# Optimization experiments

Measured on AMD Instinct MI355X. Metric: run time of the kernel, lower is better.

## Reference

```python
import jax, jax.numpy as jnp
import numpy as np

# ---- static config (mirrors module init / config constants) ----
STATE_DIM = 512
D_H = 2048
INPUT_DIM = 1024
N_QUBITS = 6
N_VQC_LAYERS = 3
MSD = 128                 # mamba_state_dim (last dim of padded state)
PAD_SLICES = 16           # padded slice count in h_padded
MIN_T = 1e-6              # control_limits.min_value
REL_STEP = 0.1            # control_limits.hardware_relative_step
ABS_STEP = 1e-4           # control_limits.hardware_absolute_step
MAX_T = 0.05              # control_limits.max_value
DIM = 2 ** N_QUBITS

# qubit 0 = most significant bit (matches reshape-based gate application)
_BITS = ((np.arange(DIM)[:, None] >> np.arange(N_QUBITS)[None, ::-1]) & 1).astype(np.float32)
_sign = np.ones(DIM, np.float32)
for k in range(N_QUBITS):  # ring CZ entanglement
    k2 = (k + 1) % N_QUBITS
    _sign *= 1.0 - 2.0 * _BITS[:, k] * _BITS[:, k2]
CZ_SIGN = jnp.asarray(_sign)
Z_OBS = jnp.asarray((1.0 - 2.0 * _BITS).mean(axis=1))  # mean <Z_k> observable weights


def _apply_ry(state, ang, k):
    # state: [B, 2^n] real statevector; ang: [B] rotation angle on qubit k
    B = state.shape[0]
    s = state.reshape(B, 2 ** k, 2, 2 ** (N_QUBITS - k - 1))
    c = jnp.cos(ang / 2)[:, None, None]
    si = jnp.sin(ang / 2)[:, None, None]
    a0, a1 = s[:, :, 0, :], s[:, :, 1, :]
    out = jnp.stack([c * a0 - si * a1, si * a0 + c * a1], axis=2)
    return out.reshape(B, DIM)


def _vqc(feats, enc_W, enc_b, thetas):
    # EvolutionTimeVQCLayer: angle-encode features, layered RY + ring CZ, mean-Z expectation
    B = feats.shape[0]
    angles = feats @ enc_W + enc_b  # [B, n_qubits]
    state = jnp.zeros((B, DIM), feats.dtype).at[:, 0].set(1.0)
    for k in range(N_QUBITS):
        state = _apply_ry(state, angles[:, k], k)
    for l in range(N_VQC_LAYERS):
        for k in range(N_QUBITS):
            state = _apply_ry(state, jnp.broadcast_to(thetas[l, k], (B,)), k)
        state = state * CZ_SIGN[None, :]
    return (state * state) @ Z_OBS  # [B]


def _hamiltonian(q, p, x, W1, b1, W2, b2, W3, b3):
    z = jnp.concatenate([q, p, x], axis=-1)          # [B, 2*S + D]
    h1 = jnp.tanh(z @ W1 + b1)
    h2 = jnp.tanh(h1 @ W2 + b2)
    return (h2 @ W3)[:, 0] + b3                       # [B] scalar energy per sample


def setup_inputs() -> dict:
    key = jax.random.key(0)
    ks = jax.random.split(key, 12)
    def glorot(k, shape):
        std = np.sqrt(2.0 / (shape[0] + shape[-1]))
        return jax.random.normal(k, shape, jnp.float32) * std
    B = 2048
    h_in = 2 * STATE_DIM + INPUT_DIM
    gen_in = INPUT_DIM + 2 * STATE_DIM
    return {
        'x': jax.random.normal(ks[0], (B, INPUT_DIM), jnp.float32),
        'h_padded': jax.random.normal(ks[1], (B, PAD_SLICES, MSD), jnp.float32),
        'aux_padded': jnp.zeros((B, PAD_SLICES, MSD), jnp.float32),
        'W1': glorot(ks[2], (h_in, D_H)), 'b1': jnp.zeros((D_H,), jnp.float32),
        'W2': glorot(ks[3], (D_H, D_H)), 'b2': jnp.zeros((D_H,), jnp.float32),
        'W3': glorot(ks[4], (D_H, 1)), 'b3': jnp.zeros((), jnp.float32),
        'W_out': glorot(ks[5], (2 * STATE_DIM, INPUT_DIM)),
        'b_out': jnp.zeros((INPUT_DIM,), jnp.float32),
        'enc_W': glorot(ks[6], (gen_in, N_QUBITS)) * 0.1,
        'enc_b': jnp.zeros((N_QUBITS,), jnp.float32),
        'thetas': jax.random.normal(ks[7], (N_VQC_LAYERS, N_QUBITS), jnp.float32) * 0.1,
        'gain': jnp.asarray(0.1, jnp.float32),
        'shift': jnp.asarray(7.0, jnp.float32),
        'cap_param': jnp.asarray(0.02, jnp.float32),
        'time_bias': jnp.asarray(0.0005, jnp.float32),
        'last_stable': jnp.asarray(0.0005, jnp.float32),
    }


def reference(x, h_padded, aux_padded, W1, b1, W2, b2, W3, b3, W_out, b_out,
              enc_W, enc_b, thetas, gain, shift, cap_param, time_bias, last_stable):
    B = x.shape[0]
    total = 2 * STATE_DIM
    num_slices = total // MSD
    # unpack phase-space state from padded mamba-shaped state
    unpacked = h_padded[:, :num_slices, :].reshape(B, total)
    q_t, p_t = jnp.split(unpacked, 2, axis=-1)

    # ---- evolution-time generation via VQC ----
    ctrl = jnp.concatenate([x, q_t, p_t], axis=-1)
    samples = _vqc(ctrl, enc_W, enc_b, thetas)                       # [B]
    soft_gain = jax.nn.softplus(gain)
    soft_shift = jax.nn.softplus(shift)
    adjusted = jax.nn.softplus(soft_gain * samples - soft_shift)
    raw = jnp.mean(adjusted) + time_bias
    cap = jnp.maximum(jax.nn.softplus(cap_param), 1e-6)
    evo = cap * jax.nn.sigmoid(raw / cap)
    evo = jnp.where(jnp.isfinite(evo), evo, cap * jax.nn.sigmoid(time_bias / cap))
    prev = jnp.maximum(last_stable, MIN_T)
    cand = jnp.maximum(evo, MIN_T)
    max_step = jnp.maximum(prev * REL_STEP, ABS_STEP)
    cand = jnp.minimum(cand, prev + max_step)
    cand = jnp.minimum(cand, MAX_T)
    dt = jnp.where(jnp.isfinite(cand), cand, prev)                   # scalar

    # ---- fused HNN symplectic (leapfrog) step ----
    def H_sum(q, p):
        return _hamiltonian(q, p, x, W1, b1, W2, b2, W3, b3).sum()
    grad_qp = jax.grad(H_sum, argnums=(0, 1))
    dHdq0, _ = grad_qp(q_t, p_t)
    p_half = p_t - 0.5 * dt * dHdq0
    _, dHdp_h = grad_qp(q_t, p_half)
    q_next = q_t + dt * dHdp_h
    dHdq_n, _ = grad_qp(q_next, p_half)
    p_next = p_half - 0.5 * dt * dHdq_n

    out = jnp.concatenate([q_next, p_next], axis=-1) @ W_out + b_out  # [B, INPUT_DIM]

    # repack state into padded mamba layout
    new_slices = jnp.concatenate([q_next, p_next], axis=-1).reshape(B, num_slices, MSD)
    pad = jnp.zeros((B, PAD_SLICES - num_slices, MSD), out.dtype)
    h_next = jnp.concatenate([new_slices, pad], axis=1)
    return out, h_next
```

## Files before the change

kernel.cpp:

```cpp
#include <hip/hip_runtime.h>
#include <math.h>

#define NB 2048
#define ZD 2048
#define SD 512
#define NELEM_Z (NB * ZD)
#define MB_ (1024 * 1024)

typedef float f32x4 __attribute__((ext_vector_type(4)));
typedef __bf16 bf16x8 __attribute__((ext_vector_type(8)));
typedef __bf16 bf16x4 __attribute__((ext_vector_type(4)));
typedef int i32x4 __attribute__((ext_vector_type(4)));
typedef int i32x8 __attribute__((ext_vector_type(8)));
typedef long long i64;

__device__ __forceinline__ float softplus_f(float x) {
  if (x > 20.f) return x;
  if (x < -20.f) return expf(x);
  return log1pf(expf(x));
}

__device__ __forceinline__ void gload_lds16(const __bf16* g, __bf16* l) {
  __builtin_amdgcn_global_load_lds(
      (__attribute__((address_space(1))) void*)(g),
      (__attribute__((address_space(3))) void*)(l), 16, 0, 0);
}

__device__ __forceinline__ int pack_fp8x4(float a, float b, float c, float d) {
  int p = __builtin_amdgcn_cvt_pk_fp8_f32(a, b, 0, false);
  p = __builtin_amdgcn_cvt_pk_fp8_f32(c, d, p, true);
  return p;
}
__device__ __forceinline__ float fp8_to_f32(unsigned char b) {
  return __builtin_amdgcn_cvt_f32_fp8((int)b, 0);
}

__global__ __launch_bounds__(256) void build_z_kernel(
    const float* __restrict__ x,
    const float* __restrict__ h_padded,
    const float* __restrict__ enc_W,
    const float* __restrict__ enc_b,
    float* __restrict__ z,
    __bf16* __restrict__ zb,
    unsigned char* __restrict__ zf8,
    float* __restrict__ angles) {
  int b = blockIdx.x;
  int tid = threadIdx.x;
  int lane = tid & 63, w = tid >> 6;
  __shared__ float red[4][6];

  float pa[6] = {0.f, 0.f, 0.f, 0.f, 0.f, 0.f};
#pragma unroll
  for (int cc = 0; cc < 2; cc++) {
    int c = cc * 256 + tid;
    int i = c * 4;
    f32x4 v = (i < 1024) ? ((const f32x4*)(h_padded + (size_t)b * 2048))[c]
                         : ((const f32x4*)(x + (size_t)b * 1024))[c - 256];
    size_t zi = (size_t)b * 512 + c;
    ((f32x4*)z)[zi] = v;
    bf16x4 o;
    o[0] = (__bf16)v[0]; o[1] = (__bf16)v[1];
    o[2] = (__bf16)v[2]; o[3] = (__bf16)v[3];
    ((bf16x4*)zb)[zi] = o;
    ((int*)zf8)[zi] = pack_fp8x4(v[0], v[1], v[2], v[3]);
    int cj = (i < 1024) ? (1024 + i) : (i - 1024);
#pragma unroll
    for (int e = 0; e < 4; e++) {
      const float* wp = enc_W + (size_t)(cj + e) * 6;
#pragma unroll
      for (int k = 0; k < 6; k++) pa[k] += v[e] * wp[k];
    }
  }
#pragma unroll
  for (int k = 0; k < 6; k++)
    for (int off = 32; off > 0; off >>= 1) pa[k] += __shfl_down(pa[k], off, 64);
  if (lane == 0) {
#pragma unroll
    for (int k = 0; k < 6; k++) red[w][k] = pa[k];
  }
  __syncthreads();
  if (tid < 6)
    angles[b * 6 + tid] =
        red[0][tid] + red[1][tid] + red[2][tid] + red[3][tid] + enc_b[tid];
}

__global__ void prep_w(const float* __restrict__ in,
                       __bf16* __restrict__ outT, int R, int C) {
  __shared__ float tile[32][33];
  int bx = blockIdx.x * 32, by = blockIdx.y * 32;
  int tx = threadIdx.x, ty = threadIdx.y;
  for (int r = ty; r < 32; r += 8)
    tile[r][tx] = in[(size_t)(by + r) * C + bx + tx];
  __syncthreads();
  for (int r = ty; r < 32; r += 8)
    outT[(size_t)(bx + r) * R + by + tx] = (__bf16)tile[tx][r];
}

__global__ void prep_w8(const float* __restrict__ in,
                        unsigned char* __restrict__ outN,
                        unsigned char* __restrict__ outT, int R, int C) {
  __shared__ float tile[32][33];
  int bx = blockIdx.x * 32, by = blockIdx.y * 32;
  int tx = threadIdx.x, ty = threadIdx.y;
  for (int r = ty; r < 32; r += 8) {
    float v = in[(size_t)(by + r) * C + bx + tx] * 16.f;
    tile[r][tx] = v;
    int p = __builtin_amdgcn_cvt_pk_fp8_f32(v, v, 0, false);
    outN[(size_t)(by + r) * C + bx + tx] = (unsigned char)(p & 0xff);
  }
  __syncthreads();
  for (int r = ty; r < 32; r += 8) {
    float v = tile[tx][r];
    int p = __builtin_amdgcn_cvt_pk_fp8_f32(v, v, 0, false);
    outT[(size_t)(bx + r) * R + by + tx] = (unsigned char)(p & 0xff);
  }
}

__global__ __launch_bounds__(256) void sim_kernel(
    const float* __restrict__ angles,
    const float* __restrict__ thetas,
    const float* __restrict__ gain,
    const float* __restrict__ shift,
    float* __restrict__ partial) {
  const int lane = threadIdx.x & 63;
  const int wv = threadIdx.x >> 6;
  const int row = blockIdx.x * 4 + wv;

  const int rot = ((lane << 1) | (lane >> 5)) & 63;
  const float czs = (__popc(lane & rot) & 1) ? -1.f : 1.f;
  const float zo = (6.f - 2.f * (float)__popc(lane)) * (1.f / 6.f);

  float ang = 0.f;
  if (lane < 6) ang = angles[row * 6 + lane];
  else if (lane < 24) ang = thetas[lane - 6];
  float half = 0.5f * ang;
  float cj = cosf(half), sj = sinf(half);

  float c_arr[24], s_arr[24];
#pragma unroll
  for (int j = 0; j < 24; j++) {
    c_arr[j] = __shfl(cj, j, 64);
    s_arr[j] = __shfl(sj, j, 64);
  }

  float s = (lane == 0) ? 1.f : 0.f;
#pragma unroll
  for (int j = 0; j < 24; j++) {
    const int m = 1 << (5 - (j % 6));
    float t = __shfl_xor(s, m, 64);
    float tt = (lane & m) ? t : -t;
    s = fmaf(c_arr[j], s, s_arr[j] * tt);
    if (j >= 6 && (j % 6) == 5) s *= czs;
  }

  float val = s * s * zo;
#pragma unroll
  for (int off = 32; off > 0; off >>= 1) val += __shfl_xor(val, off, 64);

  __shared__ float red[4];
  if (lane == 0) {
    float sg = softplus_f(gain[0]);
    float ss = softplus_f(shift[0]);
    red[wv] = softplus_f(sg * val - ss);
  }
  __syncthreads();
  if (threadIdx.x == 0)
    partial[blockIdx.x] = red[0] + red[1] + red[2] + red[3];
}

__global__ __launch_bounds__(256) void dt_kernel(
    const float* __restrict__ partial,
    const float* __restrict__ cap_param,
    const float* __restrict__ time_bias,
    const float* __restrict__ last_stable,
    float* __restrict__ dt_out) {
  int tid = threadIdx.x;
  int lane = tid & 63, wv = tid >> 6;
  float v = partial[tid] + partial[tid + 256];
#pragma unroll
  for (int off = 32; off > 0; off >>= 1) v += __shfl_xor(v, off, 64);
  __shared__ float red[4];
  if (lane == 0) red[wv] = v;
  __syncthreads();
  if (tid == 0) {
    float a = red[0] + red[1] + red[2] + red[3];
    float raw = a * (1.f / (float)NB) + time_bias[0];
    float cap = fmaxf(softplus_f(cap_param[0]), 1e-6f);
    float evo = cap / (1.f + expf(-raw / cap));
    if (!isfinite(evo)) evo = cap / (1.f + expf(-time_bias[0] / cap));
    float prev = fmaxf(last_stable[0], 1e-6f);
    float cand = fmaxf(evo, 1e-6f);
    float max_step = fmaxf(prev * 0.1f, 1e-4f);
    cand = fminf(cand, prev + max_step);
    cand = fminf(cand, 0.05f);
    dt_out[0] = isfinite(cand) ? cand : prev;
  }
}

template <int EPI>
__global__ __launch_bounds__(256, 2) void mfma_gemm8(
    const unsigned char* __restrict__ A, int lda,
    const unsigned char* __restrict__ Bt, int ldb,
    void* __restrict__ Cv, int ldc,
    const float* __restrict__ bias,
    const float* __restrict__ w3,
    const unsigned char* __restrict__ aux, int ldaux,
    int Kslice) {
  __shared__ __align__(16) unsigned char sA[2][128 * 128];
  __shared__ __align__(16) unsigned char sB[2][64 * 128];

  const int tid = threadIdx.x;
  const int lane = tid & 63;
  const int w = tid >> 6;
  const int wm = w & 1, wn = w >> 1;
  const int row0 = blockIdx.y * 128;
  const int col0 = blockIdx.x * 64;
  const int koff = blockIdx.z * Kslice;

  const unsigned char* gA[4]; int wA[4];
  const unsigned char* gB[2]; int wB[2];
#pragma unroll
  for (int i = 0; i < 4; i++) {
    int c = i * 256 + tid;
    int m = c >> 3, s = c & 7;
    gA[i] = A + (size_t)(row0 + m) * lda + koff + s * 16;
    wA[i] = m * 128 + ((s ^ (m & 7)) << 4);
  }
#pragma unroll
  for (int i = 0; i < 2; i++) {
    int c = i * 256 + tid;
    int m = c >> 3, s = c & 7;
    gB[i] = Bt + (size_t)(col0 + m) * ldb + koff + s * 16;
    wB[i] = m * 128 + ((s ^ (m & 7)) << 4);
  }

  const int q = lane >> 4, r = lane & 15;
  int aoff[4][2], boff[2][2];
#pragma unroll
  for (int i = 0; i < 4; i++) {
    int ma = wm * 64 + i * 16 + r;
#pragma unroll
    for (int H = 0; H < 2; H++)
      aoff[i][H] = ma * 128 + (((2 * q + H) ^ (ma & 7)) << 4);
  }
#pragma unroll
  for (int j = 0; j < 2; j++) {
    int mb = wn * 32 + j * 16 + r;
#pragma unroll
    for (int H = 0; H < 2; H++)
      boff[j][H] = mb * 128 + (((2 * q + H) ^ (mb & 7)) << 4);
  }

  f32x4 acc[4][2] = {};
  f32x4 rA[4], rB[2];

#pragma unroll
  for (int i = 0; i < 4; i++) rA[i] = *(const f32x4*)gA[i];
#pragma unroll
  for (int i = 0; i < 2; i++) rB[i] = *(const f32x4*)gB[i];
#pragma unroll
  for (int i = 0; i < 4; i++) *(f32x4*)(&sA[0][0] + wA[i]) = rA[i];
#pragma unroll
  for (int i = 0; i < 2; i++) *(f32x4*)(&sB[0][0] + wB[i]) = rB[i];
  __syncthreads();

  int cur = 0;
  for (int k0 = 0; k0 < Kslice; k0 += 128) {
    const bool more = (k0 + 128 < Kslice);
    if (more) {
#pragma unroll
      for (int i = 0; i < 4; i++) rA[i] = *(const f32x4*)(gA[i] + k0 + 128);
#pragma unroll
      for (int i = 0; i < 2; i++) rB[i] = *(const f32x4*)(gB[i] + k0 + 128);
    }

    const unsigned char* bA = &sA[cur][0];
    const unsigned char* bB = &sB[cur][0];
    i32x8 af[4], bfr[2];
#pragma unroll
    for (int i = 0; i < 4; i++) {
      i32x4 lo = *(const i32x4*)(bA + aoff[i][0]);
      i32x4 hi = *(const i32x4*)(bA + aoff[i][1]);
      af[i] = __builtin_shufflevector(lo, hi, 0, 1, 2, 3, 4, 5, 6, 7);
    }
#pragma unroll
    for (int j = 0; j < 2; j++) {
      i32x4 lo = *(const i32x4*)(bB + boff[j][0]);
      i32x4 hi = *(const i32x4*)(bB + boff[j][1]);
      bfr[j] = __builtin_shufflevector(lo, hi, 0, 1, 2, 3, 4, 5, 6, 7);
    }
#pragma unroll
    for (int i = 0; i < 4; i++)
#pragma unroll
      for (int j = 0; j < 2; j++)
        acc[i][j] = __builtin_amdgcn_mfma_scale_f32_16x16x128_f8f6f4(
            af[i], bfr[j], acc[i][j], 0 , 0 ,
            0, 0x7F7F7F7F, 0, 0x7F7F7F7F);

    if (more) {
      unsigned char* nA = &sA[cur ^ 1][0];
      unsigned char* nB = &sB[cur ^ 1][0];
#pragma unroll
      for (int i = 0; i < 4; i++) *(f32x4*)(nA + wA[i]) = rA[i];
#pragma unroll
      for (int i = 0; i < 2; i++) *(f32x4*)(nB + wB[i]) = rB[i];
    }
    __syncthreads();
    cur ^= 1;
  }

  float* Cf = (float*)Cv;
  unsigned char* C8 = (unsigned char*)Cv;
  float* Pz = Cf + (size_t)blockIdx.z * (size_t)gridDim.y * 128 * ldc;

#pragma unroll
  for (int i = 0; i < 4; i++) {
    int rowb = row0 + wm * 64 + i * 16 + q * 4;
#pragma unroll
    for (int j = 0; j < 2; j++) {
      int col = col0 + wn * 32 + j * 16 + r;
      if (EPI == 0) {
#pragma unroll
        for (int g = 0; g < 4; g++)
          Pz[(size_t)(rowb + g) * ldc + col] = acc[i][j][g];
      } else {
        float o[4];
#pragma unroll
        for (int g = 0; g < 4; g++) {
          float v = acc[i][j][g] * 0.0625f;
          if (EPI == 1) {
            o[g] = tanhf(v + bias[col]);
          } else if (EPI == 2) {
            float t = tanhf(v + bias[col]);
            o[g] = 32.f * (1.f - t * t) * w3[col];
          } else {
            float h = fp8_to_f32(aux[(size_t)(rowb + g) * ldaux + col]);
            o[g] = v * (1.f - h * h);
          }
        }
        int p = pack_fp8x4(o[0], o[1], o[2], o[3]);
#pragma unroll
        for (int g = 0; g < 4; g++)
          C8[(size_t)(rowb + g) * ldc + col] =
              (unsigned char)((p >> (8 * g)) & 0xff);
      }
    }
  }
}

__global__ __launch_bounds__(256, 2) void mfma_gemm_bf16(
    const __bf16* __restrict__ A, int lda,
    const __bf16* __restrict__ Bt, int ldb,
    float* __restrict__ P, int ldc,
    int Kslice) {
  __shared__ __bf16 sA[2][128 * 64];
  __shared__ __bf16 sB[2][64 * 64];

  const int tid = threadIdx.x;
  const int lane = tid & 63;
  const int w = tid >> 6;
  const int wm = w & 1, wn = w >> 1;
  const int row0 = blockIdx.y * 128;
  const int col0 = blockIdx.x * 64;
  const int koff = blockIdx.z * Kslice;

  const __bf16* gA[4]; int lofA[4];
  const __bf16* gB[2]; int lofB[2];
#pragma unroll
  for (int i = 0; i < 4; i++) {
    int c = i * 256 + tid;
    int m = c >> 3, cc = c & 7;
    int o = cc ^ (m & 7);
    gA[i] = A + (size_t)(row0 + m) * lda + koff + o * 8;
    lofA[i] = c * 8;
  }
#pragma unroll
  for (int i = 0; i < 2; i++) {
    int c = i * 256 + tid;
    int m = c >> 3, cc = c & 7;
    int o = cc ^ (m & 7);
    gB[i] = Bt + (size_t)(col0 + m) * ldb + koff + o * 8;
    lofB[i] = c * 8;
  }

  const int q = lane >> 4, r = lane & 15;
  int aoff[4][2], boff[2][2];
#pragma unroll
  for (int i = 0; i < 4; i++) {
    int ma = wm * 64 + i * 16 + r;
#pragma unroll
    for (int h = 0; h < 2; h++)
      aoff[i][h] = (ma * 8 + ((h * 4 + q) ^ (ma & 7))) * 8;
  }
#pragma unroll
  for (int j = 0; j < 2; j++) {
    int mb = wn * 32 + j * 16 + r;
#pragma unroll
    for (int h = 0; h < 2; h++)
      boff[j][h] = (mb * 8 + ((h * 4 + q) ^ (mb & 7))) * 8;
  }

  f32x4 acc[4][2] = {};

#pragma unroll
  for (int i = 0; i < 4; i++) gload_lds16(gA[i], &sA[0][0] + lofA[i]);
#pragma unroll
  for (int i = 0; i < 2; i++) gload_lds16(gB[i], &sB[0][0] + lofB[i]);

  int cur = 0;
  for (int k0 = 0; k0 < Kslice; k0 += 64) {
    __syncthreads();
    if (k0 + 64 < Kslice) {
      int nxt = cur ^ 1;
#pragma unroll
      for (int i = 0; i < 4; i++)
        gload_lds16(gA[i] + k0 + 64, &sA[nxt][0] + lofA[i]);
#pragma unroll
      for (int i = 0; i < 2; i++)
        gload_lds16(gB[i] + k0 + 64, &sB[nxt][0] + lofB[i]);
    }
#pragma unroll
    for (int h = 0; h < 2; h++) {
      bf16x8 af[4], bfr[2];
#pragma unroll
      for (int i = 0; i < 4; i++)
        af[i] = *(const bf16x8*)(&sA[cur][0] + aoff[i][h]);
#pragma unroll
      for (int j = 0; j < 2; j++)
        bfr[j] = *(const bf16x8*)(&sB[cur][0] + boff[j][h]);
#pragma unroll
      for (int i = 0; i < 4; i++)
#pragma unroll
        for (int j = 0; j < 2; j++)
          acc[i][j] = __builtin_amdgcn_mfma_f32_16x16x32_bf16(af[i], bfr[j],
                                                              acc[i][j], 0, 0, 0);
    }
    cur ^= 1;
  }

  float* Pz = P + (size_t)blockIdx.z * (size_t)gridDim.y * 128 * ldc;
#pragma unroll
  for (int i = 0; i < 4; i++) {
    int rowb = row0 + wm * 64 + i * 16 + q * 4;
#pragma unroll
    for (int j = 0; j < 2; j++) {
      int col = col0 + wn * 32 + j * 16 + r;
#pragma unroll
      for (int g = 0; g < 4; g++)
        Pz[(size_t)(rowb + g) * ldc + col] = acc[i][j][g];
    }
  }
}

__global__ void update_kernel(float* __restrict__ z, __bf16* __restrict__ zb,
                              unsigned char* __restrict__ zf8,
                              const float* __restrict__ gp,
                              const float* __restrict__ dt,
                              float coef, int off) {
  int t = blockIdx.x * blockDim.x + threadIdx.x;
  int b = t >> 7;
  int j4 = t & 127;
  const f32x4* g4 = (const f32x4*)gp;
  constexpr int STRIDE = NB * SD / 4;
  f32x4 g = g4[t] + g4[t + STRIDE] + g4[t + 2 * STRIDE] + g4[t + 3 * STRIDE];
  int zi4 = (b * ZD + off) / 4 + j4;
  f32x4 v = ((f32x4*)z)[zi4];
  float s = coef * dt[0] * (1.f / 512.f);
  v[0] += s * g[0]; v[1] += s * g[1]; v[2] += s * g[2]; v[3] += s * g[3];
  ((f32x4*)z)[zi4] = v;
  bf16x4 o;
  o[0] = (__bf16)v[0]; o[1] = (__bf16)v[1];
  o[2] = (__bf16)v[2]; o[3] = (__bf16)v[3];
  ((bf16x4*)zb)[zi4] = o;
  ((int*)zf8)[zi4] = pack_fp8x4(v[0], v[1], v[2], v[3]);
}

__global__ void wout_reduce(const float* __restrict__ gp,
                            const float* __restrict__ b_out,
                            float* __restrict__ out) {
  int t = blockIdx.x * blockDim.x + threadIdx.x;
  constexpr int S = NB * 1024 / 4;
  const f32x4* g4 = (const f32x4*)gp;
  f32x4 v = g4[t] + g4[t + S];
  f32x4 bb = ((const f32x4*)b_out)[t & 255];
  v[0] += bb[0]; v[1] += bb[1]; v[2] += bb[2]; v[3] += bb[3];
  ((f32x4*)out)[t] = v;
}

__global__ void hnext_kernel(const float* __restrict__ z,
                             float* __restrict__ out) {
  int t = blockIdx.x * blockDim.x + threadIdx.x;
  int i4 = t & 511;
  f32x4 zero = {0.f, 0.f, 0.f, 0.f};
  ((f32x4*)out)[t] = (i4 < 256) ? ((const f32x4*)z)[t] : zero;
}

extern "C" void kernel_launch(void* const* d_in, const int* in_sizes, int n_in,
                              void* d_out, int out_size, void* d_ws,
                              size_t ws_size, hipStream_t stream) {
  const float* x        = (const float*)d_in[0];
  const float* h_padded = (const float*)d_in[1];
  const float* W1    = (const float*)d_in[3];
  const float* b1    = (const float*)d_in[4];
  const float* W2    = (const float*)d_in[5];
  const float* b2    = (const float*)d_in[6];
  const float* W3    = (const float*)d_in[7];
  const float* W_out = (const float*)d_in[9];
  const float* b_out = (const float*)d_in[10];
  const float* enc_W = (const float*)d_in[11];
  const float* enc_b = (const float*)d_in[12];
  const float* thetas = (const float*)d_in[13];
  const float* gain   = (const float*)d_in[14];
  const float* shift  = (const float*)d_in[15];
  const float* cap_p  = (const float*)d_in[16];
  const float* t_bias = (const float*)d_in[17];
  const float* l_stab = (const float*)d_in[18];

  float* out_mat  = (float*)d_out;
  float* out_hnxt = (float*)d_out + NB * 1024;

  char* base = (char*)d_ws;
  float* z      = (float*)(base);
  float* part   = (float*)(base + 16 * MB_);
  __bf16* zb    = (__bf16*)(base + 32 * MB_);
  __bf16* Wot   = (__bf16*)(base + 40 * MB_);
  float* angl   = (float*)(base + 42 * MB_);
  float* accp   = (float*)(base + 42 * MB_ + 65536);
  float* dtp    = accp + 1;
  float* simp   = (float*)(base + 42 * MB_ + 80 * 1024);
  unsigned char* zf8  = (unsigned char*)(base + 43 * MB_);
  unsigned char* h1_8 = zf8 + (size_t)NELEM_Z;
  unsigned char* g2_8 = h1_8 + (size_t)NELEM_Z;
  unsigned char* g1_8 = g2_8 + (size_t)NELEM_Z;
  unsigned char* W1n8 = g1_8 + (size_t)NELEM_Z;
  unsigned char* W1t8 = W1n8 + (size_t)NELEM_Z;
  unsigned char* W2n8 = W1t8 + (size_t)NELEM_Z;
  unsigned char* W2t8 = W2n8 + (size_t)NELEM_Z;

  dim3 thr256(256);
  dim3 thrT(32, 8);

  prep_w8<<<dim3(64, 64), thrT, 0, stream>>>(W1, W1n8, W1t8, ZD, ZD);
  prep_w8<<<dim3(64, 64), thrT, 0, stream>>>(W2, W2n8, W2t8, ZD, ZD);
  prep_w<<<dim3(32, 32), thrT, 0, stream>>>(W_out, Wot, 1024, 1024);

  build_z_kernel<<<dim3(NB), thr256, 0, stream>>>(x, h_padded, enc_W, enc_b, z,
                                                  zb, zf8, angl);
  sim_kernel<<<dim3(NB / 4), thr256, 0, stream>>>(angl, thetas, gain, shift,
                                                  simp);
  dt_kernel<<<dim3(1), thr256, 0, stream>>>(simp, cap_p, t_bias, l_stab, dtp);

  const int   j0r[3]  = {0, 512, 0};
  const int   offs[3] = {512, 0, 512};
  const float coef[3] = {-0.5f, 1.0f, -0.5f};

  dim3 gridSq(32, 16, 1);
  dim3 gridGr(8, 16, 4);

  for (int i = 0; i < 3; i++) {
    mfma_gemm8<1><<<gridSq, thr256, 0, stream>>>(
        zf8, ZD, W1t8, ZD, h1_8, ZD, b1, nullptr, nullptr, 0, ZD);
    mfma_gemm8<2><<<gridSq, thr256, 0, stream>>>(
        h1_8, ZD, W2t8, ZD, g2_8, ZD, b2, W3, nullptr, 0, ZD);
    mfma_gemm8<3><<<gridSq, thr256, 0, stream>>>(
        g2_8, ZD, W2n8, ZD, g1_8, ZD, nullptr, nullptr, h1_8, ZD, ZD);
    mfma_gemm8<0><<<gridGr, thr256, 0, stream>>>(
        g1_8, ZD, W1n8 + (size_t)j0r[i] * ZD, ZD, part, SD, nullptr, nullptr,
        nullptr, 0, 512);
    update_kernel<<<dim3(NB * SD / 4 / 256), thr256, 0, stream>>>(
        z, zb, zf8, part, dtp, coef[i], offs[i]);
  }

  mfma_gemm_bf16<<<dim3(16, 16, 2), thr256, 0, stream>>>(zb, ZD, Wot, 1024,
                                                         part, 1024, 512);
  wout_reduce<<<dim3(NB * 1024 / 4 / 256), thr256, 0, stream>>>(part, b_out,
                                                                out_mat);

  hnext_kernel<<<dim3(NELEM_Z / 4 / 256), thr256, 0, stream>>>(z, out_hnxt);
}
```

Baseline: 412.1 us.

## Widen FP8 GEMM tile to 128x128 and stage operands with direct global-to-LDS loads

The FP8 MFMA GEMM tile grows from 128x64 to 128x128 outputs per block, so each wave computes a 4x4 grid of 16x16 MFMA tiles and operand reuse improves. Launch grids are halved to match. Global-to-register-to-LDS staging is replaced by global_load_lds direct copies, with the XOR swizzle moved to the global source address, and the barrier moved to the top of the loop. The costs are twice the LDS per block, more accumulator registers, and only about one block per CU, which may leave little latency hiding.

```diff
diff --git a/kernel.cpp b/kernel.cpp
--- a/kernel.cpp
+++ b/kernel.cpp
@@ -21,6 +21,12 @@
 }
 
 __device__ __forceinline__ void gload_lds16(const __bf16* g, __bf16* l) {
+  __builtin_amdgcn_global_load_lds(
+      (__attribute__((address_space(1))) void*)(g),
+      (__attribute__((address_space(3))) void*)(l), 16, 0, 0);
+}
+__device__ __forceinline__ void gload_lds16u(const unsigned char* g,
+                                             unsigned char* l) {
   __builtin_amdgcn_global_load_lds(
       (__attribute__((address_space(1))) void*)(g),
       (__attribute__((address_space(3))) void*)(l), 16, 0, 0);
@@ -207,35 +213,31 @@
     const unsigned char* __restrict__ aux, int ldaux,
     int Kslice) {
   __shared__ __align__(16) unsigned char sA[2][128 * 128];
-  __shared__ __align__(16) unsigned char sB[2][64 * 128];
+  __shared__ __align__(16) unsigned char sB[2][128 * 128];
 
   const int tid = threadIdx.x;
   const int lane = tid & 63;
   const int w = tid >> 6;
   const int wm = w & 1, wn = w >> 1;
   const int row0 = blockIdx.y * 128;
-  const int col0 = blockIdx.x * 64;
+  const int col0 = blockIdx.x * 128;
   const int koff = blockIdx.z * Kslice;
 
-  const unsigned char* gA[4]; int wA[4];
-  const unsigned char* gB[2]; int wB[2];
+  const unsigned char* gA[4];
+  const unsigned char* gB[4];
+  int ldst[4];
 #pragma unroll
   for (int i = 0; i < 4; i++) {
     int c = i * 256 + tid;
     int m = c >> 3, s = c & 7;
-    gA[i] = A + (size_t)(row0 + m) * lda + koff + s * 16;
-    wA[i] = m * 128 + ((s ^ (m & 7)) << 4);
-  }
-#pragma unroll
-  for (int i = 0; i < 2; i++) {
-    int c = i * 256 + tid;
-    int m = c >> 3, s = c & 7;
-    gB[i] = Bt + (size_t)(col0 + m) * ldb + koff + s * 16;
-    wB[i] = m * 128 + ((s ^ (m & 7)) << 4);
+    int l = s ^ (m & 7);
+    gA[i] = A + (size_t)(row0 + m) * lda + koff + l * 16;
+    gB[i] = Bt + (size_t)(col0 + m) * ldb + koff + l * 16;
+    ldst[i] = c * 16;
   }
 
   const int q = lane >> 4, r = lane & 15;
-  int aoff[4][2], boff[2][2];
+  int aoff[4][2], boff[4][2];
 #pragma unroll
   for (int i = 0; i < 4; i++) {
     int ma = wm * 64 + i * 16 + r;
@@ -244,39 +246,36 @@
       aoff[i][H] = ma * 128 + (((2 * q + H) ^ (ma & 7)) << 4);
   }
 #pragma unroll
-  for (int j = 0; j < 2; j++) {
-    int mb = wn * 32 + j * 16 + r;
+  for (int j = 0; j < 4; j++) {
+    int mb = wn * 64 + j * 16 + r;
 #pragma unroll
     for (int H = 0; H < 2; H++)
       boff[j][H] = mb * 128 + (((2 * q + H) ^ (mb & 7)) << 4);
   }
 
-  f32x4 acc[4][2] = {};
-  f32x4 rA[4], rB[2];
-
-#pragma unroll
-  for (int i = 0; i < 4; i++) rA[i] = *(const f32x4*)gA[i];
-#pragma unroll
-  for (int i = 0; i < 2; i++) rB[i] = *(const f32x4*)gB[i];
-#pragma unroll
-  for (int i = 0; i < 4; i++) *(f32x4*)(&sA[0][0] + wA[i]) = rA[i];
-#pragma unroll
-  for (int i = 0; i < 2; i++) *(f32x4*)(&sB[0][0] + wB[i]) = rB[i];
-  __syncthreads();
+  f32x4 acc[4][4] = {};
+
+#pragma unroll
+  for (int i = 0; i < 4; i++) gload_lds16u(gA[i], &sA[0][0] + ldst[i]);
+#pragma unroll
+  for (int i = 0; i < 4; i++) gload_lds16u(gB[i], &sB[0][0] + ldst[i]);
 
   int cur = 0;
   for (int k0 = 0; k0 < Kslice; k0 += 128) {
-    const bool more = (k0 + 128 < Kslice);
-    if (more) {
-#pragma unroll
-      for (int i = 0; i < 4; i++) rA[i] = *(const f32x4*)(gA[i] + k0 + 128);
-#pragma unroll
-      for (int i = 0; i < 2; i++) rB[i] = *(const f32x4*)(gB[i] + k0 + 128);
+    __syncthreads();
+    if (k0 + 128 < Kslice) {
+      int nxt = cur ^ 1;
+#pragma unroll
+      for (int i = 0; i < 4; i++)
+        gload_lds16u(gA[i] + k0 + 128, &sA[nxt][0] + ldst[i]);
+#pragma unroll
+      for (int i = 0; i < 4; i++)
+        gload_lds16u(gB[i] + k0 + 128, &sB[nxt][0] + ldst[i]);
     }
 
     const unsigned char* bA = &sA[cur][0];
     const unsigned char* bB = &sB[cur][0];
-    i32x8 af[4], bfr[2];
+    i32x8 af[4], bfr[4];
 #pragma unroll
     for (int i = 0; i < 4; i++) {
       i32x4 lo = *(const i32x4*)(bA + aoff[i][0]);
@@ -284,7 +283,7 @@
       af[i] = __builtin_shufflevector(lo, hi, 0, 1, 2, 3, 4, 5, 6, 7);
     }
 #pragma unroll
-    for (int j = 0; j < 2; j++) {
+    for (int j = 0; j < 4; j++) {
       i32x4 lo = *(const i32x4*)(bB + boff[j][0]);
       i32x4 hi = *(const i32x4*)(bB + boff[j][1]);
       bfr[j] = __builtin_shufflevector(lo, hi, 0, 1, 2, 3, 4, 5, 6, 7);
@@ -292,20 +291,10 @@
 #pragma unroll
     for (int i = 0; i < 4; i++)
 #pragma unroll
-      for (int j = 0; j < 2; j++)
+      for (int j = 0; j < 4; j++)
         acc[i][j] = __builtin_amdgcn_mfma_scale_f32_16x16x128_f8f6f4(
             af[i], bfr[j], acc[i][j], 0 , 0 ,
             0, 0x7F7F7F7F, 0, 0x7F7F7F7F);
-
-    if (more) {
-      unsigned char* nA = &sA[cur ^ 1][0];
-      unsigned char* nB = &sB[cur ^ 1][0];
-#pragma unroll
-      for (int i = 0; i < 4; i++) *(f32x4*)(nA + wA[i]) = rA[i];
-#pragma unroll
-      for (int i = 0; i < 2; i++) *(f32x4*)(nB + wB[i]) = rB[i];
-    }
-    __syncthreads();
     cur ^= 1;
   }
 
@@ -317,8 +306,8 @@
   for (int i = 0; i < 4; i++) {
     int rowb = row0 + wm * 64 + i * 16 + q * 4;
 #pragma unroll
-    for (int j = 0; j < 2; j++) {
-      int col = col0 + wn * 32 + j * 16 + r;
+    for (int j = 0; j < 4; j++) {
+      int col = col0 + wn * 64 + j * 16 + r;
       if (EPI == 0) {
 #pragma unroll
         for (int g = 0; g < 4; g++)
@@ -554,8 +543,8 @@
   const int   offs[3] = {512, 0, 512};
   const float coef[3] = {-0.5f, 1.0f, -0.5f};
 
-  dim3 gridSq(32, 16, 1);
-  dim3 gridGr(8, 16, 4);
+  dim3 gridSq(16, 16, 1);
+  dim3 gridGr(4, 16, 4);
 
   for (int i = 0; i < 3; i++) {
     mfma_gemm8<1><<<gridSq, thr256, 0, stream>>>(
```

Result: slower. 468.7 us (+13.7%).

## Replace scaled 16x16x128 fp8 MFMA with 16x16x32 fp8 MFMA and padded LDS

Applied to the files above, without the earlier changes.

Switches the fp8 GEMM inner product from the gfx950 scaled 16x16x128 f8f6f4 MFMA to four 16x16x32 fp8 MFMAs per K-step. The shared-memory tiles move from an XOR swizzle to a padded 144-byte row stride, with 8-byte interleaved stores so each lane's 16-byte read supplies two consecutive K=32 operands. This likely trades the wider instruction for more MFMA issues and twice as many narrower LDS stores. The likely aim is a simpler or more conflict-free LDS layout, at the cost of using the older, lower-throughput MFMA instruction.

```diff
diff --git a/kernel.cpp b/kernel.cpp
--- a/kernel.cpp
+++ b/kernel.cpp
@@ -10,8 +10,6 @@
 typedef float f32x4 __attribute__((ext_vector_type(4)));
 typedef __bf16 bf16x8 __attribute__((ext_vector_type(8)));
 typedef __bf16 bf16x4 __attribute__((ext_vector_type(4)));
-typedef int i32x4 __attribute__((ext_vector_type(4)));
-typedef int i32x8 __attribute__((ext_vector_type(8)));
 typedef long long i64;
 
 __device__ __forceinline__ float softplus_f(float x) {
@@ -206,8 +204,8 @@
     const float* __restrict__ w3,
     const unsigned char* __restrict__ aux, int ldaux,
     int Kslice) {
-  __shared__ __align__(16) unsigned char sA[2][128 * 128];
-  __shared__ __align__(16) unsigned char sB[2][64 * 128];
+  __shared__ __align__(16) unsigned char sA[2][128 * 144];
+  __shared__ __align__(16) unsigned char sB[2][64 * 144];
 
   const int tid = threadIdx.x;
   const int lane = tid & 63;
@@ -217,21 +215,27 @@
   const int col0 = blockIdx.x * 64;
   const int koff = blockIdx.z * Kslice;
 
-  const unsigned char* gA[4]; int wA[4];
-  const unsigned char* gB[2]; int wB[2];
+  const unsigned char* gA[4]; int wA0[4], wA1[4];
+  const unsigned char* gB[2]; int wB0[2], wB1[2];
 #pragma unroll
   for (int i = 0; i < 4; i++) {
     int c = i * 256 + tid;
-    int m = c >> 3, s = c & 7;
-    gA[i] = A + (size_t)(row0 + m) * lda + koff + s * 16;
-    wA[i] = m * 128 + ((s ^ (m & 7)) << 4);
+    int m = c >> 3, cp = c & 7;
+    gA[i] = A + (size_t)(row0 + m) * lda + koff + cp * 16;
+    int h = cp >> 1;
+    int Hofs = (h >> 1) * 16 + (h & 1) * 8;
+    wA0[i] = m * 144 + ((2 * cp) & 3) * 32 + Hofs;
+    wA1[i] = m * 144 + ((2 * cp + 1) & 3) * 32 + Hofs;
   }
 #pragma unroll
   for (int i = 0; i < 2; i++) {
     int c = i * 256 + tid;
-    int m = c >> 3, s = c & 7;
-    gB[i] = Bt + (size_t)(col0 + m) * ldb + koff + s * 16;
-    wB[i] = m * 128 + ((s ^ (m & 7)) << 4);
+    int m = c >> 3, cp = c & 7;
+    gB[i] = Bt + (size_t)(col0 + m) * ldb + koff + cp * 16;
+    int h = cp >> 1;
+    int Hofs = (h >> 1) * 16 + (h & 1) * 8;
+    wB0[i] = m * 144 + ((2 * cp) & 3) * 32 + Hofs;
+    wB1[i] = m * 144 + ((2 * cp + 1) & 3) * 32 + Hofs;
   }
 
   const int q = lane >> 4, r = lane & 15;
@@ -240,15 +244,13 @@
   for (int i = 0; i < 4; i++) {
     int ma = wm * 64 + i * 16 + r;
 #pragma unroll
-    for (int H = 0; H < 2; H++)
-      aoff[i][H] = ma * 128 + (((2 * q + H) ^ (ma & 7)) << 4);
+    for (int H = 0; H < 2; H++) aoff[i][H] = ma * 144 + q * 32 + H * 16;
   }
 #pragma unroll
   for (int j = 0; j < 2; j++) {
     int mb = wn * 32 + j * 16 + r;
 #pragma unroll
-    for (int H = 0; H < 2; H++)
-      boff[j][H] = mb * 128 + (((2 * q + H) ^ (mb & 7)) << 4);
+    for (int H = 0; H < 2; H++) boff[j][H] = mb * 144 + q * 32 + H * 16;
   }
 
   f32x4 acc[4][2] = {};
@@ -259,9 +261,15 @@
 #pragma unroll
   for (int i = 0; i < 2; i++) rB[i] = *(const f32x4*)gB[i];
 #pragma unroll
-  for (int i = 0; i < 4; i++) *(f32x4*)(&sA[0][0] + wA[i]) = rA[i];
-#pragma unroll
-  for (int i = 0; i < 2; i++) *(f32x4*)(&sB[0][0] + wB[i]) = rB[i];
+  for (int i = 0; i < 4; i++) {
+    *(i64*)(&sA[0][0] + wA0[i]) = ((const i64*)&rA[i])[0];
+    *(i64*)(&sA[0][0] + wA1[i]) = ((const i64*)&rA[i])[1];
+  }
+#pragma unroll
+  for (int i = 0; i < 2; i++) {
+    *(i64*)(&sB[0][0] + wB0[i]) = ((const i64*)&rB[i])[0];
+    *(i64*)(&sB[0][0] + wB1[i]) = ((const i64*)&rB[i])[1];
+  }
   __syncthreads();
 
   int cur = 0;
@@ -276,34 +284,48 @@
 
     const unsigned char* bA = &sA[cur][0];
     const unsigned char* bB = &sB[cur][0];
-    i32x8 af[4], bfr[2];
-#pragma unroll
-    for (int i = 0; i < 4; i++) {
-      i32x4 lo = *(const i32x4*)(bA + aoff[i][0]);
-      i32x4 hi = *(const i32x4*)(bA + aoff[i][1]);
-      af[i] = __builtin_shufflevector(lo, hi, 0, 1, 2, 3, 4, 5, 6, 7);
-    }
-#pragma unroll
-    for (int j = 0; j < 2; j++) {
-      i32x4 lo = *(const i32x4*)(bB + boff[j][0]);
-      i32x4 hi = *(const i32x4*)(bB + boff[j][1]);
-      bfr[j] = __builtin_shufflevector(lo, hi, 0, 1, 2, 3, 4, 5, 6, 7);
-    }
-#pragma unroll
-    for (int i = 0; i < 4; i++)
-#pragma unroll
-      for (int j = 0; j < 2; j++)
-        acc[i][j] = __builtin_amdgcn_mfma_scale_f32_16x16x128_f8f6f4(
-            af[i], bfr[j], acc[i][j], 0 , 0 ,
-            0, 0x7F7F7F7F, 0, 0x7F7F7F7F);
+#pragma unroll
+    for (int H = 0; H < 2; H++) {
+      i64 a0[4], a1[4], b0[2], b1[2];
+#pragma unroll
+      for (int i = 0; i < 4; i++) {
+        f32x4 v = *(const f32x4*)(bA + aoff[i][H]);
+        a0[i] = ((const i64*)&v)[0];
+        a1[i] = ((const i64*)&v)[1];
+      }
+#pragma unroll
+      for (int j = 0; j < 2; j++) {
+        f32x4 v = *(const f32x4*)(bB + boff[j][H]);
+        b0[j] = ((const i64*)&v)[0];
+        b1[j] = ((const i64*)&v)[1];
+      }
+#pragma unroll
+      for (int i = 0; i < 4; i++)
+#pragma unroll
+        for (int j = 0; j < 2; j++)
+          acc[i][j] = __builtin_amdgcn_mfma_f32_16x16x32_fp8_fp8(
+              a0[i], b0[j], acc[i][j], 0, 0, 0);
+#pragma unroll
+      for (int i = 0; i < 4; i++)
+#pragma unroll
+        for (int j = 0; j < 2; j++)
+          acc[i][j] = __builtin_amdgcn_mfma_f32_16x16x32_fp8_fp8(
+              a1[i], b1[j], acc[i][j], 0, 0, 0);
+    }
 
     if (more) {
       unsigned char* nA = &sA[cur ^ 1][0];
       unsigned char* nB = &sB[cur ^ 1][0];
 #pragma unroll
-      for (int i = 0; i < 4; i++) *(f32x4*)(nA + wA[i]) = rA[i];
-#pragma unroll
-      for (int i = 0; i < 2; i++) *(f32x4*)(nB + wB[i]) = rB[i];
+      for (int i = 0; i < 4; i++) {
+        *(i64*)(nA + wA0[i]) = ((const i64*)&rA[i])[0];
+        *(i64*)(nA + wA1[i]) = ((const i64*)&rA[i])[1];
+      }
+#pragma unroll
+      for (int i = 0; i < 2; i++) {
+        *(i64*)(nB + wB0[i]) = ((const i64*)&rB[i])[0];
+        *(i64*)(nB + wB1[i]) = ((const i64*)&rB[i])[1];
+      }
     }
     __syncthreads();
     cur ^= 1;
```

Result: slower. 429.2 us (+4.2%).
